# Performance work log

Measured on AMD Instinct MI355X. Metric: run time of the kernel, lower is better.

The kernel has to match this reference:

```python
import jax, jax.numpy as jnp
import numpy as np

T, B, IN, H, E = 100, 1, 36, 256, 2048


def setup_inputs() -> dict:
    key = jax.random.key(0)
    ks = jax.random.split(key, 18)
    rn = lambda k, shape, s=1.0: jax.random.normal(k, shape, jnp.float32) * s
    return dict(
        Y=rn(ks[0], (T, B, IN)),
        h0=rn(ks[1], (1, B, H)),
        c0=rn(ks[2], (1, B, H)),
        outEncoder=rn(ks[3], (E, H), 0.1),
        W_ih=rn(ks[4], (4 * H, IN), 0.1),
        W_hh=rn(ks[5], (4 * H, H), 0.1),
        b_ih=rn(ks[6], (4 * H,), 0.1),
        b_hh=rn(ks[7], (4 * H,), 0.1),
        att_W=rn(ks[8], (H, H), 0.1),
        att_V=rn(ks[9], (H, H), 0.1),
        att_b=rn(ks[10], (H, 1), 0.1),
        att_vector=rn(ks[11], (1, H), 0.1),
        W1=rn(ks[12], (H, 2 * H), 0.1),
        b1=rn(ks[13], (H,), 0.1),
        W2=rn(ks[14], (H, H), 0.1),
        b2=rn(ks[15], (H,), 0.1),
        W3=rn(ks[16], (IN, H), 0.1),
        b3=rn(ks[17], (IN,), 0.1),
    )


def reference(Y, h0, c0, outEncoder, W_ih, W_hh, b_ih, b_hh,
              att_W, att_V, att_b, att_vector, W1, b1, W2, b2, W3, b3):
    h = jnp.squeeze(h0, 0)  # [B,H]
    c = jnp.squeeze(c0, 0)  # [B,H]
    # VOut = att_V @ outEncoder^T is timestep-invariant: precompute. [H,E]
    VOut = att_V @ outEncoder.T

    def step(carry, y):
        h, c = carry  # h: [B,H], c: [B,H] (context from prev step after step 0)
        gates = y @ W_ih.T + b_ih + h @ W_hh.T + b_hh  # [B,4H]
        i_g, f_g, g_g, o_g = jnp.split(gates, 4, axis=1)
        cLSTM = jax.nn.sigmoid(f_g) * c + jax.nn.sigmoid(i_g) * jnp.tanh(g_g)
        h_new = jax.nn.sigmoid(o_g) * jnp.tanh(cLSTM)  # [B,H]
        # additive attention: hidden expanded to every encoder position
        WS = att_W @ h_new.T  # [H,1], broadcasts over E columns
        Escore = jnp.tanh(WS + VOut + att_b)  # [H,E]
        scores = att_vector @ Escore  # [1,E]
        alpha = jax.nn.softmax(scores, axis=-1)  # [1,E]
        ctx = alpha @ outEncoder  # [1,H]
        # MLP on concat(new cell state, context)
        v = jnp.concatenate([cLSTM, ctx], axis=1)  # [1,2H]
        v = jax.nn.relu(v @ W1.T + b1)
        v = jax.nn.relu(v @ W2.T + b2)
        out = v @ W3.T + b3  # [1,36]
        # NB: original feeds the attention context back as the LSTM cell state
        return (h_new, ctx), out

    (_, c_final), outputs = jax.lax.scan(step, (h, c), Y)
    return outputs, c_final  # outputs: [100,1,36]
```

## Files before the change

### kernel.cpp

```cpp
#include <hip/hip_runtime.h>
#include <stdint.h>


static constexpr float    L2E = 1.44269504088896341f;
static constexpr float    K2  = 2.88539008177792681f;
static constexpr unsigned SPIN_LIMIT = 200000u;

static constexpr size_t OFF_BC   = 0;
static constexpr size_t OFF_YG   = 524288;
static constexpr size_t OFF_GRAW = 626688;
static constexpr size_t OFF_CRAW = 729088;
static constexpr size_t OFF_STOT = 933888;
static constexpr size_t OFF_CLH  = 937088;
static constexpr size_t OFF_V1   = 962688;
static constexpr size_t OFF_V2   = 988288;
static constexpr size_t OFF_SYNC = 1013888;

__device__ __forceinline__ float exp2fast(float x){ return __builtin_amdgcn_exp2f(x); }
__device__ __forceinline__ float rcpfast(float x){ return __builtin_amdgcn_rcpf(x); }
__device__ __forceinline__ float sigf(float x){ return rcpfast(1.f + exp2fast(-x*L2E)); }
__device__ __forceinline__ float tanhfast(float x){
  float E = exp2fast(x*K2);
  return 1.f - 2.f*rcpfast(E + 1.f);
}
__device__ __forceinline__ unsigned short f2bf(float f){
  unsigned b = __float_as_uint(f);
  return (unsigned short)((b + 0x7FFFu + ((b>>16)&1u))>>16);
}
__device__ __forceinline__ float bf2f(unsigned short u){ return __uint_as_float(((unsigned)u)<<16); }

__device__ __forceinline__ void gstore(float* p, float v){
  __hip_atomic_store(p, v, __ATOMIC_RELAXED, __HIP_MEMORY_SCOPE_AGENT);
}
__device__ __forceinline__ void gstore_u32(unsigned* p, unsigned v){
  __hip_atomic_store(p, v, __ATOMIC_RELAXED, __HIP_MEMORY_SCOPE_AGENT);
}
__device__ __forceinline__ unsigned gload_u32(const unsigned* p){
  return __hip_atomic_load(p, __ATOMIC_RELAXED, __HIP_MEMORY_SCOPE_AGENT);
}
__device__ __forceinline__ void gatomic_addf(float* p, float v){
  (void)__hip_atomic_fetch_add(p, v, __ATOMIC_RELAXED, __HIP_MEMORY_SCOPE_AGENT);
}

__device__ __forceinline__ void fbar(unsigned* flags, int w, unsigned ep){
  asm volatile("s_waitcnt vmcnt(0)" ::: "memory");
  __syncthreads();
  if (threadIdx.x == 0) gstore_u32(&flags[w], ep);
  if (threadIdx.x < 64) {
    int lane = threadIdx.x;
    unsigned it = 0;
    for (;;) {
      unsigned v = (lane < 32) ? gload_u32(&flags[lane]) : ep;
      if (__all((int)(v >= ep))) break;
      if (++it > SPIN_LIMIT) break;
    }
  }
  __syncthreads();
  asm volatile("" ::: "memory");
}
__device__ __forceinline__ void fwait_sleep(unsigned* flags, unsigned ep){
  if (threadIdx.x < 64) {
    int lane = threadIdx.x;
    unsigned it = 0;
    for (;;) {
      unsigned v = (lane < 32) ? gload_u32(&flags[lane]) : ep;
      if (__all((int)(v >= ep))) break;
      __builtin_amdgcn_s_sleep(2);
      if (++it > SPIN_LIMIT) break;
    }
  }
  __syncthreads();
  asm volatile("" ::: "memory");
}
__device__ __forceinline__ void arrive_cnt(unsigned* cnt){
  asm volatile("s_waitcnt vmcnt(0)" ::: "memory");
  __syncthreads();
  if (threadIdx.x == 0)
    __hip_atomic_fetch_add(cnt, 1u, __ATOMIC_RELAXED, __HIP_MEMORY_SCOPE_AGENT);
}
__device__ __forceinline__ void poll_ge(unsigned* p, unsigned tgt){
  if (threadIdx.x == 0){
    unsigned it = 0;
    while (gload_u32(p) < tgt){
      __builtin_amdgcn_s_sleep(2);
      if (++it > SPIN_LIMIT) break;
    }
  }
  __syncthreads();
  asm volatile("" ::: "memory");
}

__global__ __launch_bounds__(256) void rnn_prep(
    const float* __restrict__ Y, const float* __restrict__ h0,
    const float* __restrict__ outE, const float* __restrict__ W_ih,
    const float* __restrict__ W_hh, const float* __restrict__ b_ih,
    const float* __restrict__ b_hh, const float* __restrict__ att_V,
    const float* __restrict__ att_b, float* __restrict__ ws)
{
  __shared__ float avT[32*257];
  __shared__ float oeL[8*257];
  __shared__ float yL[40];
  __shared__ float h0L[256];
  const int b = blockIdx.x, tid = threadIdx.x;
  float* ws_bc   = ws + OFF_BC;
  float* ws_yg   = ws + OFF_YG;
  float* ws_graw = ws + OFF_GRAW;

  if (b < 256) {
    int e0 = b*8;
    for (int r=0;r<8;r++) oeL[r*257 + tid] = outE[(size_t)(e0+r)*256 + tid];
    int hl = tid & 31, er = tid >> 5;
    for (int ht=0; ht<8; ++ht) {
      __syncthreads();
      for (int i=0;i<32;i++){ int lin = tid + i*256; int r = lin>>8, j = lin&255;
        avT[r*257 + j] = att_V[(size_t)(ht*32+r)*256 + j]; }
      __syncthreads();
      float acc = 0.f;
      for (int j=0;j<256;j++) acc = fmaf(avT[hl*257 + j], oeL[er*257 + j], acc);
      int h = ht*32 + hl;
      ws_bc[(size_t)(e0+er)*256 + h] = (acc + att_b[h]) * K2;
    }
  } else if (b < 260) {
    int g = b - 256;
    for (int u=0; u<25; ++u) {
      int t = g*25 + u;
      __syncthreads();
      if (tid < 36) yL[tid] = Y[t*36 + tid];
      __syncthreads();
      for (int q=0;q<4;q++){
        int i = tid + 256*q;
        float acc = b_ih[i] + b_hh[i];
        for (int j=0;j<36;j++) acc = fmaf(W_ih[(size_t)i*36 + j], yL[j], acc);
        ws_yg[(size_t)t*1024 + i] = acc;
      }
    }
  } else if (b < 292) {
    int s = b - 260;
    if (tid < 256) h0L[tid] = h0[tid];
    if (tid < 36)  yL[tid]  = Y[tid];
    __syncthreads();
    int r = tid>>3, l8 = tid&7;
    int R = s*32 + r;
    float acc = 0.f;
    for (int q=0;q<32;q++){ int j = l8*32 + q; acc = fmaf(W_hh[(size_t)R*256 + j], h0L[j], acc); }
    acc += __shfl_xor(acc,1); acc += __shfl_xor(acc,2); acc += __shfl_xor(acc,4);
    if (l8 == 0){
      float full = acc + b_ih[R] + b_hh[R];
      for (int j=0;j<36;j++) full = fmaf(W_ih[(size_t)R*36 + j], yL[j], full);
      ws_graw[R] = full;
    }
  } else if (b == 292) {
    unsigned* s0 = (unsigned*)(ws + OFF_SYNC);
    s0[tid] = 0u; s0[tid + 256] = 0u;
  } else if (b == 293) {
    for (int k=0;k<13;k++){ int i = tid + k*256; if (i < 3200) ws[OFF_STOT + i] = 0.f; }
  } else {
    int t = b - 294;
    for (int k=0;k<8;k++) ws[OFF_CRAW + (size_t)t*2048 + tid + k*256] = 0.f;
  }
}

__global__ __launch_bounds__(512, 1) void rnn_main(
    const float* __restrict__ c0, const float* __restrict__ outE,
    const float* __restrict__ W_hh, const float* __restrict__ att_W,
    const float* __restrict__ att_vec,
    const float* __restrict__ W1, const float* __restrict__ b1,
    const float* __restrict__ W2, const float* __restrict__ b2,
    const float* __restrict__ W3, const float* __restrict__ b3,
    float* __restrict__ out, float* __restrict__ ws)
{
  __shared__ __align__(16) unsigned char smem[140288];
  const int w = blockIdx.x;
  const int tid = threadIdx.x;

  float* ws_yg    = ws + OFF_YG;
  float* ws_graw  = ws + OFF_GRAW;
  float* ws_craw  = ws + OFF_CRAW;
  float* ws_stotp = ws + OFF_STOT;
  float* ws_clh   = ws + OFF_CLH;
  float* ws_v1    = ws + OFF_V1;
  float* ws_v2    = ws + OFF_V2;
  unsigned* flags = (unsigned*)(ws + OFF_SYNC);
  unsigned* fv1   = flags + 64;
  unsigned* fv2   = flags + 192;

  if (w < 32) {
    float*          bcS    = (float*)(smem);
    unsigned short* oeS    = (unsigned short*)(smem + 67584);
    float*          whhS   = (float*)(smem + 100352);
    float*          wsS    = (float*)(smem + 133632);
    float*          hS     = (float*)(smem + 134688);
    float*          scoreS = (float*)(smem + 135712);
    float*          wexpS  = (float*)(smem + 135968);
    float*          pS     = (float*)(smem + 136224);
    float*          avS    = (float*)(smem + 138272);
    float*          stS    = (float*)(smem + 139328);

    float4 awR[32];
    { int r = tid>>1, p = tid&1;
      const float4* arow = (const float4*)(att_W + (size_t)r*256 + p*128);
      #pragma unroll
      for (int q=0;q<32;q++) awR[q] = arow[q]; }
    float Vpart = 0.f;
    { int l8 = tid & 7;
      #pragma unroll
      for (int k=0;k<32;k++) Vpart += att_vec[l8*32 + k]; }

    const float* ws_bc = ws + OFF_BC;
    for (int i=0;i<32;i++){ int lin = tid + i*512; int col = lin>>8, h = lin&255;
      bcS[col*264 + h + (h>>5)] = ws_bc[(size_t)(w*64+col)*256 + h]; }
    for (int i=0;i<32;i++){ int lin = tid + i*512; int col = lin>>8, h = lin&255;
      oeS[col*256 + h] = f2bf(outE[(size_t)(w*64+col)*256 + h]); }
    for (int i=0;i<16;i++){ int lin = tid + i*512; int r = lin>>8, j = lin&255;
      whhS[r*260 + j] = W_hh[(size_t)(w*32+r)*256 + j]; }
    if (tid < 256) avS[tid + (tid>>5)] = -2.f * att_vec[tid];
    __syncthreads();

    for (int t = 0; t < 100; ++t) {
      float ig, fg, gg, og;
      float4 cv0, cv1;
      if (tid < 256) {
        const float* g = ws_graw + (size_t)t*1024;
        ig = g[tid]; fg = g[256+tid]; gg = g[512+tid]; og = g[768+tid];
        if (t > 0) {
          const float4* cp = (const float4*)(ws_craw + ((size_t)(t-1)*256 + tid)*8);
          cv0 = cp[0]; cv1 = cp[1];
        }
      }
      if (t > 0 && tid < 64) {
        float v = (tid < 32) ? ws_stotp[(size_t)(t-1)*32 + tid] : 0.f;
        #pragma unroll
        for (int d=1; d<64; d<<=1) v += __shfl_xor(v, d);
        if (tid == 0) stS[0] = v;
      }
      __syncthreads();
      if (tid < 256) {
        float c;
        if (t == 0) c = c0[tid];
        else {
          float rsum = (cv0.x+cv0.y)+(cv0.z+cv0.w) + (cv1.x+cv1.y)+(cv1.z+cv1.w);
          c = rsum * rcpfast(stS[0]);
        }
        float cl = sigf(fg)*c + sigf(ig)*tanhfast(gg);
        float hn = sigf(og)*tanhfast(cl);
        hS[tid] = hn;
        if ((tid>>3) == w) gstore(&ws_clh[(size_t)t*256 + tid], cl);
      }
      __syncthreads();
      { int r = tid>>1, p = tid&1;
        const float4* h4 = (const float4*)(hS + p*128);
        float acc = 0.f;
        #pragma unroll
        for (int i=0;i<32;i++){ float4 hv = h4[i]; float4 av = awR[i];
          acc = fmaf(av.x, hv.x, acc); acc = fmaf(av.y, hv.y, acc);
          acc = fmaf(av.z, hv.z, acc); acc = fmaf(av.w, hv.w, acc); }
        acc += __shfl_xor(acc, 1);
        if (p == 0) wsS[r + (r>>5)] = acc * K2; }
      __syncthreads();
      { int col = tid >> 3, l8 = tid & 7;
        const float* bcR = bcS + col*264 + l8*33;
        const float* wsR = wsS + l8*33;
        const float* avR = avS + l8*33;
        float acc = Vpart;
        #pragma unroll
        for (int k=0;k<32;k++){
          float E = exp2fast(bcR[k] + wsR[k]);
          acc = fmaf(avR[k], rcpfast(E + 1.f), acc);
        }
        acc += __shfl_xor(acc,1); acc += __shfl_xor(acc,2); acc += __shfl_xor(acc,4);
        if (l8 == 0) scoreS[col] = acc; }
      __syncthreads();
      if (tid < 64) {
        float ev = exp2fast(scoreS[tid] * L2E);
        wexpS[tid] = ev;
        float s = ev;
        #pragma unroll
        for (int d=1; d<64; d<<=1) s += __shfl_xor(s, d);
        if (tid == 0) gstore(&ws_stotp[(size_t)t*32 + w], s);
      }
      __syncthreads();
      { int h = tid & 255, half = tid >> 8;
        float accp = 0.f;
        #pragma unroll
        for (int i=0;i<32;i++){ int lc = half*32 + i;
          accp = fmaf(wexpS[lc], bf2f(oeS[lc*256 + h]), accp); }
        pS[half*256 + h] = accp; }
      __syncthreads();
      if (tid < 256)
        gatomic_addf(&ws_craw[((size_t)t*256 + tid)*8 + (w>>2)], pS[tid] + pS[256 + tid]);
      if (t <= 98) {
        int r32 = tid >> 4, l16 = tid & 15;
        float acc2 = 0.f;
        #pragma unroll
        for (int q=0;q<16;q++){ int j = l16 + 16*q; acc2 = fmaf(whhS[r32*260 + j], hS[j], acc2); }
        acc2 += __shfl_xor(acc2,1); acc2 += __shfl_xor(acc2,2);
        acc2 += __shfl_xor(acc2,4); acc2 += __shfl_xor(acc2,8);
        if (l16 == 0){ int R = w*32 + r32;
          gstore(&ws_graw[(size_t)(t+1)*1024 + R], acc2 + ws_yg[(size_t)(t+1)*1024 + R]); }
      }
      fbar(flags, w, (unsigned)(t+1));
    }
    if (w == 0) {
      if (tid < 64) {
        float v = (tid < 32) ? ws_stotp[(size_t)99*32 + tid] : 0.f;
        #pragma unroll
        for (int d=1; d<64; d<<=1) v += __shfl_xor(v, d);
        if (tid == 0) stS[0] = v;
      }
      __syncthreads();
      if (tid < 256) {
        const float4* cp = (const float4*)(ws_craw + ((size_t)99*256 + tid)*8);
        float4 a = cp[0], b = cp[1];
        float rsum = (a.x+a.y)+(a.z+a.w) + (b.x+b.y)+(b.z+b.w);
        out[3600 + tid] = rsum * rcpfast(stS[0]);
      }
    }
  } else if (w < 36) {
    float* wmS  = (float*)(smem);
    float* vbS  = (float*)(smem + 133632);
    float* stSm = (float*)(smem + 136000);
    int m = w - 32;
    for (int i=0;i<64;i++){ int lin = tid + i*512; int r = lin>>9, k = lin&511;
      wmS[r*520 + k + (k>>6)] = W1[(size_t)(m*64+r)*512 + k]; }
    __syncthreads();
    for (int s=0; s<100; ++s){
      fwait_sleep(flags, (unsigned)(s+1));
      if (tid < 64) {
        float v = (tid < 32) ? ws_stotp[(size_t)s*32 + tid] : 0.f;
        #pragma unroll
        for (int d=1; d<64; d<<=1) v += __shfl_xor(v, d);
        if (tid == 0) stSm[0] = v;
      }
      float rawsum = 0.f;
      if (tid >= 256) {
        int h = tid - 256;
        const float4* cp = (const float4*)(ws_craw + ((size_t)s*256 + h)*8);
        float4 a = cp[0], b = cp[1];
        rawsum = (a.x+a.y)+(a.z+a.w) + (b.x+b.y)+(b.z+b.w);
      }
      __syncthreads();
      { float val = (tid < 256) ? ws_clh[(size_t)s*256 + tid]
                                : rawsum * rcpfast(stSm[0]);
        vbS[tid + (tid>>6)] = val; }
      __syncthreads();
      int row = tid >> 3, l8 = tid & 7;
      const float* wr = wmS + row*520 + l8*65;
      const float* vr = vbS + l8*65;
      float acc = 0.f;
      #pragma unroll
      for (int q=0;q<64;q++) acc = fmaf(wr[q], vr[q], acc);
      acc += __shfl_xor(acc,1); acc += __shfl_xor(acc,2); acc += __shfl_xor(acc,4);
      if (l8 == 0){ int i = m*64 + row; gstore(&ws_v1[(size_t)s*256 + i], fmaxf(acc + b1[i], 0.f)); }
      arrive_cnt(&fv1[s]);
      __syncthreads();
    }
  } else if (w < 38) {
    float* wmS = (float*)(smem);
    float* vbS = (float*)(smem + 133632);
    int m = w - 36;
    for (int i=0;i<64;i++){ int lin = tid + i*512; int r = lin>>8, k = lin&255;
      wmS[r*260 + k + (k>>6)] = W2[(size_t)(m*128+r)*256 + k]; }
    __syncthreads();
    for (int s=0; s<100; ++s){
      poll_ge(&fv1[s], 4u);
      if (tid < 256) vbS[tid + (tid>>6)] = ws_v1[(size_t)s*256 + tid];
      __syncthreads();
      int row = tid >> 2, l4 = tid & 3;
      const float* wr = wmS + row*260 + l4*65;
      const float* vr = vbS + l4*65;
      float acc = 0.f;
      #pragma unroll
      for (int q=0;q<64;q++) acc = fmaf(wr[q], vr[q], acc);
      acc += __shfl_xor(acc,1); acc += __shfl_xor(acc,2);
      if (l4 == 0){ int i = m*128 + row; gstore(&ws_v2[(size_t)s*256 + i], fmaxf(acc + b2[i], 0.f)); }
      arrive_cnt(&fv2[s]);
      __syncthreads();
    }
  } else {
    float* wmS = (float*)(smem);
    float* vbS = (float*)(smem + 37440);
    for (int lin = tid; lin < 36*256; lin += 512){ int r = lin>>8, k = lin&255;
      wmS[r*260 + k + (k>>6)] = W3[(size_t)r*256 + k]; }
    __syncthreads();
    for (int s=0; s<100; ++s){
      poll_ge(&fv2[s], 2u);
      if (tid < 256) vbS[tid + (tid>>6)] = ws_v2[(size_t)s*256 + tid];
      __syncthreads();
      if (tid < 288) {
        int row = tid >> 3, l8 = tid & 7;
        int kb = l8*32;
        const float* wr = wmS + row*260 + kb + (kb>>6);
        const float* vr = vbS + kb + (kb>>6);
        float acc = 0.f;
        #pragma unroll
        for (int q=0;q<32;q++) acc = fmaf(wr[q], vr[q], acc);
        acc += __shfl_xor(acc,1); acc += __shfl_xor(acc,2); acc += __shfl_xor(acc,4);
        if (l8 == 0) out[s*36 + row] = acc + b3[row];
      }
      __syncthreads();
    }
  }
}

extern "C" void kernel_launch(void* const* d_in, const int* in_sizes, int n_in,
                              void* d_out, int out_size, void* d_ws, size_t ws_size,
                              hipStream_t stream) {
  (void)in_sizes; (void)n_in; (void)out_size; (void)ws_size;
  const float* Y       = (const float*)d_in[0];
  const float* h0      = (const float*)d_in[1];
  const float* c0      = (const float*)d_in[2];
  const float* outEnc  = (const float*)d_in[3];
  const float* W_ih    = (const float*)d_in[4];
  const float* W_hh    = (const float*)d_in[5];
  const float* b_ih    = (const float*)d_in[6];
  const float* b_hh    = (const float*)d_in[7];
  const float* att_W   = (const float*)d_in[8];
  const float* att_V   = (const float*)d_in[9];
  const float* att_b   = (const float*)d_in[10];
  const float* att_vec = (const float*)d_in[11];
  const float* W1      = (const float*)d_in[12];
  const float* b1      = (const float*)d_in[13];
  const float* W2      = (const float*)d_in[14];
  const float* b2      = (const float*)d_in[15];
  const float* W3      = (const float*)d_in[16];
  const float* b3      = (const float*)d_in[17];
  float* out = (float*)d_out;
  float* ws  = (float*)d_ws;

  rnn_prep<<<dim3(394), dim3(256), 0, stream>>>(Y, h0, outEnc, W_ih, W_hh, b_ih, b_hh,
                                                att_V, att_b, ws);
  rnn_main<<<dim3(39), dim3(512), 0, stream>>>(c0, outEnc, W_hh, att_W, att_vec,
                                               W1, b1, W2, b2, W3, b3, out, ws);
}
```

Baseline: 767.1 us.

## Replace per-step flag barrier with data-carrying softmax-sum slots and single atomic context buffer

Removes the epoch-flag barrier between the 32 attention blocks. Instead, each block publishes its softmax partial sum only after its context atomics have drained, and consumers poll for all 32 nonzero slots, so the data itself acts as the barrier. The context accumulator collapses from 8 striped atomic lanes to one per element. The W_hh recurrent matvec moves earlier so the next gates are published sooner, and att_W is now read from global each step instead of being held in registers. This relies on partial sums never being exactly zero, and adds atomic contention on one address per element plus extra global loads for att_W.

```diff
diff --git a/kernel.cpp b/kernel.cpp
--- a/kernel.cpp
+++ b/kernel.cpp
@@ -10,11 +10,11 @@
 static constexpr size_t OFF_YG   = 524288;
 static constexpr size_t OFF_GRAW = 626688;
 static constexpr size_t OFF_CRAW = 729088;
-static constexpr size_t OFF_STOT = 933888;
-static constexpr size_t OFF_CLH  = 937088;
-static constexpr size_t OFF_V1   = 962688;
-static constexpr size_t OFF_V2   = 988288;
-static constexpr size_t OFF_SYNC = 1013888;
+static constexpr size_t OFF_STOT = 754688;
+static constexpr size_t OFF_CLH  = 757888;
+static constexpr size_t OFF_V1   = 783488;
+static constexpr size_t OFF_V2   = 809088;
+static constexpr size_t OFF_SYNC = 834688;
 
 __device__ __forceinline__ float exp2fast(float x){ return __builtin_amdgcn_exp2f(x); }
 __device__ __forceinline__ float rcpfast(float x){ return __builtin_amdgcn_rcpf(x); }
@@ -32,8 +32,8 @@
 __device__ __forceinline__ void gstore(float* p, float v){
   __hip_atomic_store(p, v, __ATOMIC_RELAXED, __HIP_MEMORY_SCOPE_AGENT);
 }
-__device__ __forceinline__ void gstore_u32(unsigned* p, unsigned v){
-  __hip_atomic_store(p, v, __ATOMIC_RELAXED, __HIP_MEMORY_SCOPE_AGENT);
+__device__ __forceinline__ float gloadf(const float* p){
+  return __hip_atomic_load(p, __ATOMIC_RELAXED, __HIP_MEMORY_SCOPE_AGENT);
 }
 __device__ __forceinline__ unsigned gload_u32(const unsigned* p){
   return __hip_atomic_load(p, __ATOMIC_RELAXED, __HIP_MEMORY_SCOPE_AGENT);
@@ -42,32 +42,19 @@
   (void)__hip_atomic_fetch_add(p, v, __ATOMIC_RELAXED, __HIP_MEMORY_SCOPE_AGENT);
 }
 
-__device__ __forceinline__ void fbar(unsigned* flags, int w, unsigned ep){
-  asm volatile("s_waitcnt vmcnt(0)" ::: "memory");
-  __syncthreads();
-  if (threadIdx.x == 0) gstore_u32(&flags[w], ep);
-  if (threadIdx.x < 64) {
-    int lane = threadIdx.x;
-    unsigned it = 0;
-    for (;;) {
-      unsigned v = (lane < 32) ? gload_u32(&flags[lane]) : ep;
-      if (__all((int)(v >= ep))) break;
+__device__ __forceinline__ void poll_reduce_stot(const float* slots, float* stS, bool polite){
+  if (threadIdx.x < 64){
+    float v; unsigned it = 0;
+    for(;;){
+      v = (threadIdx.x < 32) ? gloadf(&slots[threadIdx.x]) : 1.0f;
+      if (__all((int)(v != 0.0f))) break;
+      if (polite) __builtin_amdgcn_s_sleep(2);
       if (++it > SPIN_LIMIT) break;
     }
-  }
-  __syncthreads();
-  asm volatile("" ::: "memory");
-}
-__device__ __forceinline__ void fwait_sleep(unsigned* flags, unsigned ep){
-  if (threadIdx.x < 64) {
-    int lane = threadIdx.x;
-    unsigned it = 0;
-    for (;;) {
-      unsigned v = (lane < 32) ? gload_u32(&flags[lane]) : ep;
-      if (__all((int)(v >= ep))) break;
-      __builtin_amdgcn_s_sleep(2);
-      if (++it > SPIN_LIMIT) break;
-    }
+    float s = (threadIdx.x < 32) ? v : 0.f;
+    #pragma unroll
+    for (int d=1; d<64; d<<=1) s += __shfl_xor(s, d);
+    if (threadIdx.x == 0) stS[0] = s;
   }
   __syncthreads();
   asm volatile("" ::: "memory");
@@ -156,7 +143,7 @@
     for (int k=0;k<13;k++){ int i = tid + k*256; if (i < 3200) ws[OFF_STOT + i] = 0.f; }
   } else {
     int t = b - 294;
-    for (int k=0;k<8;k++) ws[OFF_CRAW + (size_t)t*2048 + tid + k*256] = 0.f;
+    ws[OFF_CRAW + (size_t)t*256 + tid] = 0.f;
   }
 }
 
@@ -180,9 +167,9 @@
   float* ws_clh   = ws + OFF_CLH;
   float* ws_v1    = ws + OFF_V1;
   float* ws_v2    = ws + OFF_V2;
-  unsigned* flags = (unsigned*)(ws + OFF_SYNC);
-  unsigned* fv1   = flags + 64;
-  unsigned* fv2   = flags + 192;
+  unsigned* syncb = (unsigned*)(ws + OFF_SYNC);
+  unsigned* fv1   = syncb + 64;
+  unsigned* fv2   = syncb + 192;
 
   if (w < 32) {
     float*          bcS    = (float*)(smem);
@@ -196,11 +183,6 @@
     float*          avS    = (float*)(smem + 138272);
     float*          stS    = (float*)(smem + 139328);
 
-    float4 awR[32];
-    { int r = tid>>1, p = tid&1;
-      const float4* arow = (const float4*)(att_W + (size_t)r*256 + p*128);
-      #pragma unroll
-      for (int q=0;q<32;q++) awR[q] = arow[q]; }
     float Vpart = 0.f;
     { int l8 = tid & 7;
       #pragma unroll
@@ -217,41 +199,35 @@
     __syncthreads();
 
     for (int t = 0; t < 100; ++t) {
-      float ig, fg, gg, og;
-      float4 cv0, cv1;
+      if (t > 0) poll_reduce_stot(ws_stotp + (size_t)(t-1)*32, stS, false);
+      else       __syncthreads();
       if (tid < 256) {
         const float* g = ws_graw + (size_t)t*1024;
-        ig = g[tid]; fg = g[256+tid]; gg = g[512+tid]; og = g[768+tid];
-        if (t > 0) {
-          const float4* cp = (const float4*)(ws_craw + ((size_t)(t-1)*256 + tid)*8);
-          cv0 = cp[0]; cv1 = cp[1];
-        }
-      }
-      if (t > 0 && tid < 64) {
-        float v = (tid < 32) ? ws_stotp[(size_t)(t-1)*32 + tid] : 0.f;
-        #pragma unroll
-        for (int d=1; d<64; d<<=1) v += __shfl_xor(v, d);
-        if (tid == 0) stS[0] = v;
-      }
-      __syncthreads();
-      if (tid < 256) {
-        float c;
-        if (t == 0) c = c0[tid];
-        else {
-          float rsum = (cv0.x+cv0.y)+(cv0.z+cv0.w) + (cv1.x+cv1.y)+(cv1.z+cv1.w);
-          c = rsum * rcpfast(stS[0]);
-        }
+        float ig = g[tid], fg = g[256+tid], gg = g[512+tid], og = g[768+tid];
+        float c  = (t == 0) ? c0[tid]
+                            : ws_craw[(size_t)(t-1)*256 + tid] * rcpfast(stS[0]);
         float cl = sigf(fg)*c + sigf(ig)*tanhfast(gg);
         float hn = sigf(og)*tanhfast(cl);
         hS[tid] = hn;
         if ((tid>>3) == w) gstore(&ws_clh[(size_t)t*256 + tid], cl);
       }
       __syncthreads();
+      if (t <= 98) {
+        int r32 = tid >> 4, l16 = tid & 15;
+        float acc2 = 0.f;
+        #pragma unroll
+        for (int q=0;q<16;q++){ int j = l16 + 16*q; acc2 = fmaf(whhS[r32*260 + j], hS[j], acc2); }
+        acc2 += __shfl_xor(acc2,1); acc2 += __shfl_xor(acc2,2);
+        acc2 += __shfl_xor(acc2,4); acc2 += __shfl_xor(acc2,8);
+        if (l16 == 0){ int R = w*32 + r32;
+          gstore(&ws_graw[(size_t)(t+1)*1024 + R], acc2 + ws_yg[(size_t)(t+1)*1024 + R]); }
+      }
       { int r = tid>>1, p = tid&1;
-        const float4* h4 = (const float4*)(hS + p*128);
+        const float4* arow = (const float4*)(att_W + (size_t)r*256 + p*128);
+        const float4* h4   = (const float4*)(hS + p*128);
         float acc = 0.f;
         #pragma unroll
-        for (int i=0;i<32;i++){ float4 hv = h4[i]; float4 av = awR[i];
+        for (int i=0;i<32;i++){ float4 av = arow[i]; float4 hv = h4[i];
           acc = fmaf(av.x, hv.x, acc); acc = fmaf(av.y, hv.y, acc);
           acc = fmaf(av.z, hv.z, acc); acc = fmaf(av.w, hv.w, acc); }
         acc += __shfl_xor(acc, 1);
@@ -270,13 +246,14 @@
         acc += __shfl_xor(acc,1); acc += __shfl_xor(acc,2); acc += __shfl_xor(acc,4);
         if (l8 == 0) scoreS[col] = acc; }
       __syncthreads();
+      float mySw = 0.f;
       if (tid < 64) {
         float ev = exp2fast(scoreS[tid] * L2E);
         wexpS[tid] = ev;
         float s = ev;
         #pragma unroll
         for (int d=1; d<64; d<<=1) s += __shfl_xor(s, d);
-        if (tid == 0) gstore(&ws_stotp[(size_t)t*32 + w], s);
+        mySw = s;
       }
       __syncthreads();
       { int h = tid & 255, half = tid >> 8;
@@ -286,34 +263,15 @@
           accp = fmaf(wexpS[lc], bf2f(oeS[lc*256 + h]), accp); }
         pS[half*256 + h] = accp; }
       __syncthreads();
+      if (tid < 256) gatomic_addf(&ws_craw[(size_t)t*256 + tid], pS[tid] + pS[256 + tid]);
+      asm volatile("s_waitcnt vmcnt(0)" ::: "memory");
+      __syncthreads();
+      if (tid == 0) gstore(&ws_stotp[(size_t)t*32 + w], mySw);
+    }
+    if (w == 0) {
+      poll_reduce_stot(ws_stotp + (size_t)99*32, stS, false);
       if (tid < 256)
-        gatomic_addf(&ws_craw[((size_t)t*256 + tid)*8 + (w>>2)], pS[tid] + pS[256 + tid]);
-      if (t <= 98) {
-        int r32 = tid >> 4, l16 = tid & 15;
-        float acc2 = 0.f;
-        #pragma unroll
-        for (int q=0;q<16;q++){ int j = l16 + 16*q; acc2 = fmaf(whhS[r32*260 + j], hS[j], acc2); }
-        acc2 += __shfl_xor(acc2,1); acc2 += __shfl_xor(acc2,2);
-        acc2 += __shfl_xor(acc2,4); acc2 += __shfl_xor(acc2,8);
-        if (l16 == 0){ int R = w*32 + r32;
-          gstore(&ws_graw[(size_t)(t+1)*1024 + R], acc2 + ws_yg[(size_t)(t+1)*1024 + R]); }
-      }
-      fbar(flags, w, (unsigned)(t+1));
-    }
-    if (w == 0) {
-      if (tid < 64) {
-        float v = (tid < 32) ? ws_stotp[(size_t)99*32 + tid] : 0.f;
-        #pragma unroll
-        for (int d=1; d<64; d<<=1) v += __shfl_xor(v, d);
-        if (tid == 0) stS[0] = v;
-      }
-      __syncthreads();
-      if (tid < 256) {
-        const float4* cp = (const float4*)(ws_craw + ((size_t)99*256 + tid)*8);
-        float4 a = cp[0], b = cp[1];
-        float rsum = (a.x+a.y)+(a.z+a.w) + (b.x+b.y)+(b.z+b.w);
-        out[3600 + tid] = rsum * rcpfast(stS[0]);
-      }
+        out[3600 + tid] = ws_craw[(size_t)99*256 + tid] * rcpfast(stS[0]);
     }
   } else if (w < 36) {
     float* wmS  = (float*)(smem);
@@ -324,23 +282,9 @@
       wmS[r*520 + k + (k>>6)] = W1[(size_t)(m*64+r)*512 + k]; }
     __syncthreads();
     for (int s=0; s<100; ++s){
-      fwait_sleep(flags, (unsigned)(s+1));
-      if (tid < 64) {
-        float v = (tid < 32) ? ws_stotp[(size_t)s*32 + tid] : 0.f;
-        #pragma unroll
-        for (int d=1; d<64; d<<=1) v += __shfl_xor(v, d);
-        if (tid == 0) stSm[0] = v;
-      }
-      float rawsum = 0.f;
-      if (tid >= 256) {
-        int h = tid - 256;
-        const float4* cp = (const float4*)(ws_craw + ((size_t)s*256 + h)*8);
-        float4 a = cp[0], b = cp[1];
-        rawsum = (a.x+a.y)+(a.z+a.w) + (b.x+b.y)+(b.z+b.w);
-      }
-      __syncthreads();
+      poll_reduce_stot(ws_stotp + (size_t)s*32, stSm, true);
       { float val = (tid < 256) ? ws_clh[(size_t)s*256 + tid]
-                                : rawsum * rcpfast(stSm[0]);
+                                : ws_craw[(size_t)s*256 + (tid-256)] * rcpfast(stSm[0]);
         vbS[tid + (tid>>6)] = val; }
       __syncthreads();
       int row = tid >> 3, l8 = tid & 7;
```

New measurement: 1.358 ms. 77.0% more time.
